# Optimization experiments

Hardware: AMD Instinct MI355X
Metric: run time of the kernel (lower is better)

Reference implementation:

```python
import jax, jax.numpy as jnp
import numpy as np

B, P, N = 1024, 100, 101
EMB, H, DK = 128, 8, 16
SQRT_EMB = 11.313708498984761
CLIP = 10.0


def setup_inputs() -> dict:
    key = jax.random.key(0)
    ks = jax.random.split(key, 12)
    inp = {
        "encoded_last_node": jax.random.normal(ks[0], (B, P, EMB), jnp.float32),
        "load": jax.random.uniform(ks[1], (B, P), jnp.float32),
        "time": jax.random.uniform(ks[2], (B, P), jnp.float32),
        "length": jax.random.uniform(ks[3], (B, P), jnp.float32),
        "route_open": jax.random.uniform(ks[4], (B, P), jnp.float32),
        "ninf_mask": jnp.zeros((B, P, N), jnp.float32),
        "encoded_nodes": jax.random.normal(ks[5], (B, N, EMB), jnp.float32),
        # weights stored [in, out]
        "Wq": jax.random.normal(ks[6], (EMB + 4, H * DK), jnp.float32) * 0.05,
        "Wk": jax.random.normal(ks[7], (EMB, H * DK), jnp.float32) * 0.05,
        "Wv": jax.random.normal(ks[8], (EMB, H * DK), jnp.float32) * 0.05,
        "Wc": jax.random.normal(ks[9], (H * DK, EMB), jnp.float32) * 0.05,
        "bc": jax.random.normal(ks[10], (EMB,), jnp.float32) * 0.05,
    }
    return inp


def _heads(x):
    # [B, n, H*DK] -> [B, H, n, DK]
    b, n, _ = x.shape
    return x.reshape(b, n, H, DK).transpose(0, 2, 1, 3)


def reference(encoded_last_node, load, time, length, route_open, ninf_mask,
              encoded_nodes, Wq, Wk, Wv, Wc, bc):
    # set_kv
    k = _heads(encoded_nodes @ Wk)            # [B,H,N,DK]
    v = _heads(encoded_nodes @ Wv)            # [B,H,N,DK]
    # forward
    input_cat = jnp.concatenate(
        [encoded_last_node, load[:, :, None], time[:, :, None],
         length[:, :, None], route_open[:, :, None]], axis=2)  # [B,P,EMB+4]
    q = _heads(input_cat @ Wq)                # [B,H,P,DK]
    score = jnp.einsum('bhpd,bhnd->bhpn', q, k) / jnp.sqrt(jnp.float32(DK))
    score = score + ninf_mask[:, None, :, :]
    weights = jax.nn.softmax(score, axis=3)
    out = jnp.einsum('bhpn,bhnd->bhpd', weights, v)
    out_concat = out.transpose(0, 2, 1, 3).reshape(out.shape[0], out.shape[2], H * DK)
    mh = out_concat @ Wc + bc                 # [B,P,EMB]
    score2 = jnp.einsum('bpe,bne->bpn', mh, encoded_nodes) / SQRT_EMB
    score2 = CLIP * jnp.tanh(score2) + ninf_mask
    probs = jax.nn.softmax(score2, axis=2)
    return probs
```

## Files before the change

kernel.cpp:

```cpp
#include <hip/hip_runtime.h>
#include <stdint.h>

#define B_    1024
#define P_    100
#define N_    101
#define EMB_  128
#define H_    8
#define DK_   16

#define ROWS  112
#define KSTR  136

typedef uint16_t bf16;
typedef __attribute__((ext_vector_type(8))) short short8;
typedef __attribute__((ext_vector_type(4))) float float4v;

__device__ __forceinline__ float b2f(bf16 u) {
    union { uint32_t i; float f; } c; c.i = ((uint32_t)u) << 16; return c.f;
}
__device__ __forceinline__ bf16 f2b(float f) {
    union { float f; uint32_t i; } c; c.f = f;
    uint32_t r = (c.i + 0x7fffu + ((c.i >> 16) & 1u)) >> 16;
    return (bf16)r;
}
__device__ __forceinline__ uint32_t pk2(float a, float b) {
    return (uint32_t)f2b(a) | ((uint32_t)f2b(b) << 16);
}

__device__ __forceinline__ void stage_m(const float* __restrict__ src, int nrows,
                                        bf16* __restrict__ dst, int tid) {
    for (int i = tid; i < ROWS * 32; i += 512) {
        int r = i >> 5, c = (i & 31) << 2;
        uint32_t p0 = 0, p1 = 0;
        if (r < nrows) {
            float4 v = *(const float4*)(src + (size_t)r * EMB_ + c);
            p0 = pk2(v.x, v.y); p1 = pk2(v.z, v.w);
        }
        uint32_t* d = (uint32_t*)(dst + r * KSTR + c);
        d[0] = p0; d[1] = p1;
    }
}

__global__ __launch_bounds__(256)
void prep_wT(const float* __restrict__ Wq, const float* __restrict__ Wk,
             const float* __restrict__ Wv, const float* __restrict__ Wc,
             bf16* __restrict__ ws) {
    int idx = blockIdx.x * 256 + threadIdx.x;
    int w = idx >> 14, rem = idx & 16383;
    int k = rem >> 7, o = rem & 127;
    const float* W = (w == 0) ? Wk : (w == 1) ? Wv : (w == 2) ? Wq : Wc;
    ws[((size_t)w << 14) + o * 128 + k] = f2b(W[(size_t)k * 128 + o]);
}

__global__ __launch_bounds__(512, 2)
void vrp_kernel(const float* __restrict__ eln,
                const float* __restrict__ load_,
                const float* __restrict__ time_,
                const float* __restrict__ len_,
                const float* __restrict__ open_,
                const float* __restrict__ mask_,
                const float* __restrict__ enc_,
                const float* __restrict__ Wq,
                const float* __restrict__ bc,
                const bf16* __restrict__ wsWT,
                float* __restrict__ out)
{
    const int b    = blockIdx.x;
    const int tid  = threadIdx.x;
    const int wave = tid >> 6;
    const int lane = tid & 63;
    const int lr = lane & 15, lq = lane >> 4, lk = lq << 3;

    __shared__ bf16 smem[78336];
    __shared__ float sS4[ROWS * 4];
    __shared__ float sWq4[4 * EMB_];
    bf16* const R1 = smem;
    bf16* const R2 = smem + 15232;
    bf16* const R3 = smem + 30464;
    bf16* const R4 = smem + 47872;
    bf16* const R5 = smem + 63104;

    const bf16* WkT = wsWT;
    const bf16* WvT = wsWT + 16384;
    const bf16* WqT = wsWT + 32768;
    const bf16* WcT = wsWT + 49152;

    const float* encB  = enc_  + (size_t)b * N_ * EMB_;
    const float* elnB  = eln   + (size_t)b * P_ * EMB_;
    const float* maskB = mask_ + (size_t)b * P_ * N_;
    float*       outB  = out   + (size_t)b * P_ * N_;

    stage_m(encB, N_, R1, tid);
    stage_m(elnB, P_, R5, tid);
    {
        int d = tid >> 2, c = 112 + ((tid & 3) << 2);
        uint32_t* z = (uint32_t*)(R3 + d * KSTR + c);
        z[0] = 0; z[1] = 0;
    }
    if (tid < ROWS * 4) {
        int r = tid >> 2, j = tid & 3;
        float v = 0.f;
        if (r < P_) {
            const float* s4 = (j == 0) ? load_ : (j == 1) ? time_
                             : (j == 2) ? len_ : open_;
            v = s4[(size_t)b * P_ + r];
        }
        sS4[r * 4 + j] = v;
    }
    {
        int j = tid >> 7, c = tid & 127;
        sWq4[j * EMB_ + c] = Wq[(size_t)(EMB_ + j) * EMB_ + c];
    }
    __syncthreads();

    {
        const int col = 16 * wave + lr;
        short8 bk[4], bv[4], bq[4];
        {
            const bf16* rk = WkT + (size_t)col * 128 + lk;
            const bf16* rv = WvT + (size_t)col * 128 + lk;
            const bf16* rq = WqT + (size_t)col * 128 + lk;
            #pragma unroll
            for (int s = 0; s < 4; ++s) {
                bk[s] = *(const short8*)(rk + s * 32);
                bv[s] = *(const short8*)(rv + s * 32);
                bq[s] = *(const short8*)(rq + s * 32);
            }
        }
        #pragma unroll
        for (int mt = 0; mt < 7; ++mt) {
            short8 a[4];
            #pragma unroll
            for (int s = 0; s < 4; ++s)
                a[s] = *(const short8*)(R1 + (mt * 16 + lr) * KSTR + s * 32 + lk);
            float4v ck = {0.f, 0.f, 0.f, 0.f}, cv = {0.f, 0.f, 0.f, 0.f};
            #pragma unroll
            for (int s = 0; s < 4; ++s) {
                ck = __builtin_amdgcn_mfma_f32_16x16x32_bf16(a[s], bk[s], ck, 0, 0, 0);
                cv = __builtin_amdgcn_mfma_f32_16x16x32_bf16(a[s], bv[s], cv, 0, 0, 0);
            }
            int n0 = mt * 16 + (lq << 2);
            #pragma unroll
            for (int r = 0; r < 4; ++r)
                R2[(n0 + r) * KSTR + col] = f2b(ck[r]);
            uint32_t* d = (uint32_t*)(R3 + col * KSTR + n0);
            d[0] = pk2(cv[0], cv[1]);
            d[1] = pk2(cv[2], cv[3]);
        }
        #pragma unroll
        for (int mt = 0; mt < 7; ++mt) {
            short8 a[4];
            #pragma unroll
            for (int s = 0; s < 4; ++s)
                a[s] = *(const short8*)(R5 + (mt * 16 + lr) * KSTR + s * 32 + lk);
            float4v c = {0.f, 0.f, 0.f, 0.f};
            #pragma unroll
            for (int s = 0; s < 4; ++s)
                c = __builtin_amdgcn_mfma_f32_16x16x32_bf16(a[s], bq[s], c, 0, 0, 0);
            int row0 = mt * 16 + (lq << 2);
            float w0 = sWq4[col], w1 = sWq4[EMB_ + col];
            float w2 = sWq4[2 * EMB_ + col], w3 = sWq4[3 * EMB_ + col];
            #pragma unroll
            for (int r = 0; r < 4; ++r) {
                const float* s4 = sS4 + (row0 + r) * 4;
                float acc = c[r] + s4[0] * w0 + s4[1] * w1 + s4[2] * w2 + s4[3] * w3;
                R4[(row0 + r) * KSTR + col] = f2b(acc * 0.25f);
            }
        }
    }
    __syncthreads();

    float msk[7][4];
    if (wave < 7) {
        {
            uint32_t* z = (uint32_t*)(R1 + (wave * 16 + lr) * KSTR + 112 + (lq << 2));
            z[0] = 0; z[1] = 0;
        }
        #pragma unroll
        for (int nt = 0; nt < 7; ++nt) {
            int n = nt * 16 + lr;
            #pragma unroll
            for (int r = 0; r < 4; ++r) {
                int p = wave * 16 + (lq << 2) + r;
                float v;
                if (n >= N_) v = -3.0e38f;
                else if (p < P_) v = maskB[(size_t)p * N_ + n];
                else v = 0.f;
                msk[nt][r] = v;
            }
        }
        for (int h = 0; h < H_; ++h) {
            int k0 = (h >> 1) << 5;
            float sc[7][4];
            short8 a = *(const short8*)(R4 + (wave * 16 + lr) * KSTR + k0 + lk);
            #pragma unroll
            for (int nt = 0; nt < 7; ++nt) {
                short8 bb = *(const short8*)(R2 + (nt * 16 + lr) * KSTR + k0 + lk);
                if ((lq >> 1) != (h & 1)) bb = (short8){0,0,0,0,0,0,0,0};
                float4v cc = {0.f, 0.f, 0.f, 0.f};
                cc = __builtin_amdgcn_mfma_f32_16x16x32_bf16(a, bb, cc, 0, 0, 0);
                #pragma unroll
                for (int r = 0; r < 4; ++r) sc[nt][r] = cc[r] + msk[nt][r];
            }
            #pragma unroll
            for (int r = 0; r < 4; ++r) {
                float m = sc[0][r];
                #pragma unroll
                for (int nt = 1; nt < 7; ++nt) m = fmaxf(m, sc[nt][r]);
                #pragma unroll
                for (int d = 1; d < 16; d <<= 1) m = fmaxf(m, __shfl_xor(m, d));
                float su = 0.f;
                #pragma unroll
                for (int nt = 0; nt < 7; ++nt) {
                    float e = __expf(sc[nt][r] - m); sc[nt][r] = e; su += e;
                }
                #pragma unroll
                for (int d = 1; d < 16; d <<= 1) su += __shfl_xor(su, d);
                float inv = 1.0f / su;
                #pragma unroll
                for (int nt = 0; nt < 7; ++nt)
                    R1[(wave * 16 + (lq << 2) + r) * KSTR + nt * 16 + lr] =
                        f2b(sc[nt][r] * inv);
            }
            float4v o = {0.f, 0.f, 0.f, 0.f};
            #pragma unroll
            for (int ks = 0; ks < 128; ks += 32) {
                short8 a2 = *(const short8*)(R1 + (wave * 16 + lr) * KSTR + ks + lk);
                short8 b2 = *(const short8*)(R3 + (h * 16 + lr) * KSTR + ks + lk);
                o = __builtin_amdgcn_mfma_f32_16x16x32_bf16(a2, b2, o, 0, 0, 0);
            }
            #pragma unroll
            for (int r = 0; r < 4; ++r)
                R5[(wave * 16 + (lq << 2) + r) * KSTR + h * 16 + lr] = f2b(o[r]);
        }
    }
    __syncthreads();

    stage_m(encB, N_, R2, tid);
    {
        const int col = 16 * wave + lr;
        short8 bw[4];
        {
            const bf16* rc = WcT + (size_t)col * 128 + lk;
            #pragma unroll
            for (int s = 0; s < 4; ++s) bw[s] = *(const short8*)(rc + s * 32);
        }
        float bcv = bc[col];
        #pragma unroll
        for (int mt = 0; mt < 7; ++mt) {
            short8 a[4];
            #pragma unroll
            for (int s = 0; s < 4; ++s)
                a[s] = *(const short8*)(R5 + (mt * 16 + lr) * KSTR + s * 32 + lk);
            float4v c = {0.f, 0.f, 0.f, 0.f};
            #pragma unroll
            for (int s = 0; s < 4; ++s)
                c = __builtin_amdgcn_mfma_f32_16x16x32_bf16(a[s], bw[s], c, 0, 0, 0);
            int row0 = mt * 16 + (lq << 2);
            #pragma unroll
            for (int r = 0; r < 4; ++r) {
                float m = c[r] + bcv;
                bf16 hb = f2b(m);
                R4[(row0 + r) * KSTR + col] = hb;
                R1[(row0 + r) * KSTR + col] = f2b(m - b2f(hb));
            }
        }
    }
    __syncthreads();

    if (wave < 7) {
        short8 ahi[4], alo[4];
        #pragma unroll
        for (int s = 0; s < 4; ++s) {
            ahi[s] = *(const short8*)(R4 + (wave * 16 + lr) * KSTR + s * 32 + lk);
            alo[s] = *(const short8*)(R1 + (wave * 16 + lr) * KSTR + s * 32 + lk);
        }
        float sc[7][4];
        #pragma unroll
        for (int nt = 0; nt < 7; ++nt) {
            float4v cc = {0.f, 0.f, 0.f, 0.f};
            #pragma unroll
            for (int s = 0; s < 4; ++s) {
                short8 bb = *(const short8*)(R2 + (nt * 16 + lr) * KSTR + s * 32 + lk);
                cc = __builtin_amdgcn_mfma_f32_16x16x32_bf16(ahi[s], bb, cc, 0, 0, 0);
                cc = __builtin_amdgcn_mfma_f32_16x16x32_bf16(alo[s], bb, cc, 0, 0, 0);
            }
            #pragma unroll
            for (int r = 0; r < 4; ++r) {
                float x = cc[r] * 0.08838834764831845f;
                float t = 1.0f - 2.0f / (__expf(2.0f * x) + 1.0f);
                sc[nt][r] = 10.0f * t + msk[nt][r];
            }
        }
        #pragma unroll
        for (int r = 0; r < 4; ++r) {
            float m = sc[0][r];
            #pragma unroll
            for (int nt = 1; nt < 7; ++nt) m = fmaxf(m, sc[nt][r]);
            #pragma unroll
            for (int d = 1; d < 16; d <<= 1) m = fmaxf(m, __shfl_xor(m, d));
            float su = 0.f;
            #pragma unroll
            for (int nt = 0; nt < 7; ++nt) {
                float e = __expf(sc[nt][r] - m); sc[nt][r] = e; su += e;
            }
            #pragma unroll
            for (int d = 1; d < 16; d <<= 1) su += __shfl_xor(su, d);
            float inv = 1.0f / su;
            int p = wave * 16 + (lq << 2) + r;
            if (p < P_) {
                #pragma unroll
                for (int nt = 0; nt < 7; ++nt) {
                    int n = nt * 16 + lr;
                    if (n < N_) outB[(size_t)p * N_ + n] = sc[nt][r] * inv;
                }
            }
        }
    }
}

extern "C" void kernel_launch(void* const* d_in, const int* in_sizes, int n_in,
                              void* d_out, int out_size, void* d_ws, size_t ws_size,
                              hipStream_t stream) {
    const float* eln   = (const float*)d_in[0];
    const float* load_ = (const float*)d_in[1];
    const float* time_ = (const float*)d_in[2];
    const float* len_  = (const float*)d_in[3];
    const float* open_ = (const float*)d_in[4];
    const float* mask_ = (const float*)d_in[5];
    const float* enc_  = (const float*)d_in[6];
    const float* Wq    = (const float*)d_in[7];
    const float* Wk    = (const float*)d_in[8];
    const float* Wv    = (const float*)d_in[9];
    const float* Wc    = (const float*)d_in[10];
    const float* bc    = (const float*)d_in[11];
    float* out = (float*)d_out;
    bf16* wsWT = (bf16*)d_ws;

    prep_wT<<<dim3(256), dim3(256), 0, stream>>>(Wq, Wk, Wv, Wc, wsWT);
    vrp_kernel<<<dim3(B_), dim3(512), 0, stream>>>(
        eln, load_, time_, len_, open_, mask_, enc_, Wq, bc, wsWT, out);
}
```

Baseline: 316.2 us.

## Double block to 1024 threads and split attention heads across two wave groups

Launches 16 waves per batch element instead of 8. The projection phases are split by row tiles across the two wave halves. Attention heads are divided so 14 waves each handle four heads on separate probability buffers, with an extra barrier before the outputs are written back. The K/V/Q and Wc projections also get fused per row tile. The goal is more parallelism and latency hiding within each block, at the cost of more register pressure under launch_bounds(1024,4), more barriers, and lower occupancy per CU if registers spill.

```diff
diff --git a/kernel.cpp b/kernel.cpp
--- a/kernel.cpp
+++ b/kernel.cpp
@@ -29,7 +29,7 @@
 
 __device__ __forceinline__ void stage_m(const float* __restrict__ src, int nrows,
                                         bf16* __restrict__ dst, int tid) {
-    for (int i = tid; i < ROWS * 32; i += 512) {
+    for (int i = tid; i < ROWS * 32; i += 1024) {
         int r = i >> 5, c = (i & 31) << 2;
         uint32_t p0 = 0, p1 = 0;
         if (r < nrows) {
@@ -52,7 +52,7 @@
     ws[((size_t)w << 14) + o * 128 + k] = f2b(W[(size_t)k * 128 + o]);
 }
 
-__global__ __launch_bounds__(512, 2)
+__global__ __launch_bounds__(1024, 4)
 void vrp_kernel(const float* __restrict__ eln,
                 const float* __restrict__ load_,
                 const float* __restrict__ time_,
@@ -92,7 +92,7 @@
 
     stage_m(encB, N_, R1, tid);
     stage_m(elnB, P_, R5, tid);
-    {
+    if (tid < 512) {
         int d = tid >> 2, c = 112 + ((tid & 3) << 2);
         uint32_t* z = (uint32_t*)(R3 + d * KSTR + c);
         z[0] = 0; z[1] = 0;
@@ -107,14 +107,16 @@
         }
         sS4[r * 4 + j] = v;
     }
-    {
+    if (tid < 512) {
         int j = tid >> 7, c = tid & 127;
         sWq4[j * EMB_ + c] = Wq[(size_t)(EMB_ + j) * EMB_ + c];
     }
     __syncthreads();
 
     {
-        const int col = 16 * wave + lr;
+        const int col = 16 * (wave & 7) + lr;
+        const int mt0 = (wave >> 3) ? 4 : 0;
+        const int mt1 = (wave >> 3) ? 7 : 4;
         short8 bk[4], bv[4], bq[4];
         {
             const bf16* rk = WkT + (size_t)col * 128 + lk;
@@ -127,8 +129,9 @@
                 bq[s] = *(const short8*)(rq + s * 32);
             }
         }
-        #pragma unroll
-        for (int mt = 0; mt < 7; ++mt) {
+        float w0 = sWq4[col], w1 = sWq4[EMB_ + col];
+        float w2 = sWq4[2 * EMB_ + col], w3 = sWq4[3 * EMB_ + col];
+        for (int mt = mt0; mt < mt1; ++mt) {
             short8 a[4];
             #pragma unroll
             for (int s = 0; s < 4; ++s)
@@ -146,34 +149,33 @@
             uint32_t* d = (uint32_t*)(R3 + col * KSTR + n0);
             d[0] = pk2(cv[0], cv[1]);
             d[1] = pk2(cv[2], cv[3]);
-        }
-        #pragma unroll
-        for (int mt = 0; mt < 7; ++mt) {
-            short8 a[4];
-            #pragma unroll
-            for (int s = 0; s < 4; ++s)
-                a[s] = *(const short8*)(R5 + (mt * 16 + lr) * KSTR + s * 32 + lk);
-            float4v c = {0.f, 0.f, 0.f, 0.f};
-            #pragma unroll
-            for (int s = 0; s < 4; ++s)
-                c = __builtin_amdgcn_mfma_f32_16x16x32_bf16(a[s], bq[s], c, 0, 0, 0);
+            short8 aq[4];
+            #pragma unroll
+            for (int s = 0; s < 4; ++s)
+                aq[s] = *(const short8*)(R5 + (mt * 16 + lr) * KSTR + s * 32 + lk);
+            float4v cq = {0.f, 0.f, 0.f, 0.f};
+            #pragma unroll
+            for (int s = 0; s < 4; ++s)
+                cq = __builtin_amdgcn_mfma_f32_16x16x32_bf16(aq[s], bq[s], cq, 0, 0, 0);
             int row0 = mt * 16 + (lq << 2);
-            float w0 = sWq4[col], w1 = sWq4[EMB_ + col];
-            float w2 = sWq4[2 * EMB_ + col], w3 = sWq4[3 * EMB_ + col];
             #pragma unroll
             for (int r = 0; r < 4; ++r) {
                 const float* s4 = sS4 + (row0 + r) * 4;
-                float acc = c[r] + s4[0] * w0 + s4[1] * w1 + s4[2] * w2 + s4[3] * w3;
+                float acc = cq[r] + s4[0] * w0 + s4[1] * w1 + s4[2] * w2 + s4[3] * w3;
                 R4[(row0 + r) * KSTR + col] = f2b(acc * 0.25f);
             }
         }
     }
     __syncthreads();
 
+    const int hg = (wave >= 7) ? 1 : 0;
+    const int pt = wave - hg * 7;
     float msk[7][4];
-    if (wave < 7) {
+    float4v o4[4];
+    if (wave < 14) {
+        bf16* Pbuf = hg ? R5 : R1;
         {
-            uint32_t* z = (uint32_t*)(R1 + (wave * 16 + lr) * KSTR + 112 + (lq << 2));
+            uint32_t* z = (uint32_t*)(Pbuf + (pt * 16 + lr) * KSTR + 112 + (lq << 2));
             z[0] = 0; z[1] = 0;
         }
         #pragma unroll
@@ -181,7 +183,7 @@
             int n = nt * 16 + lr;
             #pragma unroll
             for (int r = 0; r < 4; ++r) {
-                int p = wave * 16 + (lq << 2) + r;
+                int p = pt * 16 + (lq << 2) + r;
                 float v;
                 if (n >= N_) v = -3.0e38f;
                 else if (p < P_) v = maskB[(size_t)p * N_ + n];
@@ -189,10 +191,12 @@
                 msk[nt][r] = v;
             }
         }
-        for (int h = 0; h < H_; ++h) {
+        #pragma unroll
+        for (int hh = 0; hh < 4; ++hh) {
+            int h  = hg * 4 + hh;
             int k0 = (h >> 1) << 5;
             float sc[7][4];
-            short8 a = *(const short8*)(R4 + (wave * 16 + lr) * KSTR + k0 + lk);
+            short8 a = *(const short8*)(R4 + (pt * 16 + lr) * KSTR + k0 + lk);
             #pragma unroll
             for (int nt = 0; nt < 7; ++nt) {
                 short8 bb = *(const short8*)(R2 + (nt * 16 + lr) * KSTR + k0 + lk);
@@ -219,26 +223,37 @@
                 float inv = 1.0f / su;
                 #pragma unroll
                 for (int nt = 0; nt < 7; ++nt)
-                    R1[(wave * 16 + (lq << 2) + r) * KSTR + nt * 16 + lr] =
+                    Pbuf[(pt * 16 + (lq << 2) + r) * KSTR + nt * 16 + lr] =
                         f2b(sc[nt][r] * inv);
             }
             float4v o = {0.f, 0.f, 0.f, 0.f};
             #pragma unroll
             for (int ks = 0; ks < 128; ks += 32) {
-                short8 a2 = *(const short8*)(R1 + (wave * 16 + lr) * KSTR + ks + lk);
+                short8 a2 = *(const short8*)(Pbuf + (pt * 16 + lr) * KSTR + ks + lk);
                 short8 b2 = *(const short8*)(R3 + (h * 16 + lr) * KSTR + ks + lk);
                 o = __builtin_amdgcn_mfma_f32_16x16x32_bf16(a2, b2, o, 0, 0, 0);
             }
+            o4[hh] = o;
+        }
+    }
+    __syncthreads();
+
+    if (wave < 14) {
+        #pragma unroll
+        for (int hh = 0; hh < 4; ++hh) {
+            int h = hg * 4 + hh;
             #pragma unroll
             for (int r = 0; r < 4; ++r)
-                R5[(wave * 16 + (lq << 2) + r) * KSTR + h * 16 + lr] = f2b(o[r]);
-        }
-    }
-    __syncthreads();
-
+                R4[(pt * 16 + (lq << 2) + r) * KSTR + h * 16 + lr] = f2b(o4[hh][r]);
+        }
+    }
     stage_m(encB, N_, R2, tid);
+    __syncthreads();
+
     {
-        const int col = 16 * wave + lr;
+        const int col = 16 * (wave & 7) + lr;
+        const int mt0 = (wave >> 3) ? 4 : 0;
+        const int mt1 = (wave >> 3) ? 7 : 4;
         short8 bw[4];
         {
             const bf16* rc = WcT + (size_t)col * 128 + lk;
@@ -246,12 +261,11 @@
             for (int s = 0; s < 4; ++s) bw[s] = *(const short8*)(rc + s * 32);
         }
         float bcv = bc[col];
-        #pragma unroll
-        for (int mt = 0; mt < 7; ++mt) {
+        for (int mt = mt0; mt < mt1; ++mt) {
             short8 a[4];
             #pragma unroll
             for (int s = 0; s < 4; ++s)
-                a[s] = *(const short8*)(R5 + (mt * 16 + lr) * KSTR + s * 32 + lk);
+                a[s] = *(const short8*)(R4 + (mt * 16 + lr) * KSTR + s * 32 + lk);
             float4v c = {0.f, 0.f, 0.f, 0.f};
             #pragma unroll
             for (int s = 0; s < 4; ++s)
@@ -261,8 +275,8 @@
             for (int r = 0; r < 4; ++r) {
                 float m = c[r] + bcv;
                 bf16 hb = f2b(m);
-                R4[(row0 + r) * KSTR + col] = hb;
-                R1[(row0 + r) * KSTR + col] = f2b(m - b2f(hb));
+                R1[(row0 + r) * KSTR + col] = hb;
+                R5[(row0 + r) * KSTR + col] = f2b(m - b2f(hb));
             }
         }
     }
@@ -272,8 +286,8 @@
         short8 ahi[4], alo[4];
         #pragma unroll
         for (int s = 0; s < 4; ++s) {
-            ahi[s] = *(const short8*)(R4 + (wave * 16 + lr) * KSTR + s * 32 + lk);
-            alo[s] = *(const short8*)(R1 + (wave * 16 + lr) * KSTR + s * 32 + lk);
+            ahi[s] = *(const short8*)(R1 + (pt * 16 + lr) * KSTR + s * 32 + lk);
+            alo[s] = *(const short8*)(R5 + (pt * 16 + lr) * KSTR + s * 32 + lk);
         }
         float sc[7][4];
         #pragma unroll
@@ -307,7 +321,7 @@
             #pragma unroll
             for (int d = 1; d < 16; d <<= 1) su += __shfl_xor(su, d);
             float inv = 1.0f / su;
-            int p = wave * 16 + (lq << 2) + r;
+            int p = pt * 16 + (lq << 2) + r;
             if (p < P_) {
                 #pragma unroll
                 for (int nt = 0; nt < 7; ++nt) {
@@ -338,6 +352,6 @@
     bf16* wsWT = (bf16*)d_ws;
 
     prep_wT<<<dim3(256), dim3(256), 0, stream>>>(Wq, Wk, Wv, Wc, wsWT);
-    vrp_kernel<<<dim3(B_), dim3(512), 0, stream>>>(
+    vrp_kernel<<<dim3(B_), dim3(1024), 0, stream>>>(
         eln, load_, time_, len_, open_, mask_, enc_, Wq, bc, wsWT, out);
 }
```

After: 303.8 us. 1.04x faster.
